# Optimization experiments

Measured on AMD Instinct MI355X. Metric: run time of the kernel, lower is better.

## Reference

```python
import jax, jax.numpy as jnp
import numpy as np

DIM = 512
NUM_HEADS = 8
DIM_HEAD = DIM // NUM_HEADS


def _xavier(key, shape):
    fan_in, fan_out = shape[0], shape[1]
    a = (6.0 / (fan_in + fan_out)) ** 0.5
    return jax.random.uniform(key, shape, jnp.float32, -a, a)


def setup_inputs() -> dict:
    key = jax.random.key(0)
    ks = jax.random.split(key, 8)
    B, N, M = 2, 2048, 2048
    x = jax.random.normal(ks[0], (B, N, DIM), jnp.float32)
    source = jax.random.normal(ks[1], (B, M, DIM), jnp.float32)
    source_mask = jax.random.randint(ks[2], (B, M), 0, 2) > 0
    Wq = _xavier(ks[3], (DIM, DIM)); bq = jnp.zeros((DIM,), jnp.float32)
    Wk = _xavier(ks[4], (DIM, DIM)); bk = jnp.zeros((DIM,), jnp.float32)
    Wv = _xavier(ks[5], (DIM, DIM)); bv = jnp.zeros((DIM,), jnp.float32)
    Wm = _xavier(ks[6], (DIM, DIM)); bm = jnp.zeros((DIM,), jnp.float32)
    return {"x": x, "source": source, "source_mask": source_mask,
            "Wq": Wq, "bq": bq, "Wk": Wk, "bk": bk,
            "Wv": Wv, "bv": bv, "Wm": Wm, "bm": bm}


def reference(x, source, source_mask, Wq, bq, Wk, bk, Wv, bv, Wm, bm):
    B, N, D = x.shape
    M = source.shape[-2]
    H, Dh = NUM_HEADS, DIM_HEAD
    # projections (torch Linear: x @ W^T + b)
    q = (x @ Wq.T + bq).reshape(B, N, H, Dh)
    k = (source @ Wk.T + bk).reshape(B, M, H, Dh)
    v = (source @ Wv.T + bv).reshape(B, M, H, Dh)
    scale = 1.0 / (Dh ** 0.5)
    # scores: [B, N, M, H]
    scores = jnp.einsum('bnhd,bmhd->bnmh', q, k) * scale
    scores = jnp.where(source_mask[:, None, :, None], scores, -jnp.inf)
    prob = jax.nn.softmax(scores, axis=-2)  # softmax over m
    agg = jnp.einsum('bnmh,bmhd->bnhd', prob, v).reshape(B, N, D)
    return agg @ Wm.T + bm
```

## Files before the change

kernel.cpp:

```cpp
#include <hip/hip_runtime.h>
#include <hip/hip_bf16.h>

#define DIMF 512
#define NHEAD 8
#define DHEAD 64
#define BATCH 2
#define SEQN 2048
#define SEQM 2048
#define FPS 40
#define QSCALE 0.18033688011112042f

typedef unsigned short u16;
typedef __attribute__((ext_vector_type(8))) short bf16x8;
typedef __attribute__((ext_vector_type(4))) float f32x4;

static __device__ __forceinline__ u16 f2bf(float f) {
    unsigned u = __float_as_uint(f);
    u += 0x7FFF + ((u >> 16) & 1);
    return (u16)(u >> 16);
}
static __device__ __forceinline__ u16 f2bf_fast(float f) {
    return (u16)((__float_as_uint(f) + 0x8000u) >> 16);
}

static __device__ __forceinline__
void load16(const u16* g, u16* l) {
    __builtin_amdgcn_global_load_lds(
        (const __attribute__((address_space(1))) void*)g,
        (__attribute__((address_space(3))) void*)l,
        16, 0, 0);
}

__global__ __launch_bounds__(256)
void cvt_w(const float* __restrict__ wq, const float* __restrict__ wk,
           const float* __restrict__ wv, const float* __restrict__ wm,
           const int* __restrict__ mask,
           u16* __restrict__ wqb, u16* __restrict__ wkb,
           u16* __restrict__ wvb, u16* __restrict__ wmb,
           u16* __restrict__ maskbf)
{
    int i = (blockIdx.x * 256 + threadIdx.x) * 4;
    if (blockIdx.y == 4) {
        if (i < BATCH * SEQM) {
            int4 m4 = *(const int4*)&mask[i];
            *(ushort4*)&maskbf[i] = make_ushort4(m4.x ? 0x3F80 : 0, m4.y ? 0x3F80 : 0,
                                                 m4.z ? 0x3F80 : 0, m4.w ? 0x3F80 : 0);
        }
        return;
    }
    const float* in = (blockIdx.y == 0) ? wq : (blockIdx.y == 1) ? wk
                    : (blockIdx.y == 2) ? wv : wm;
    u16* out = (blockIdx.y == 0) ? wqb : (blockIdx.y == 1) ? wkb
             : (blockIdx.y == 2) ? wvb : wmb;
    if (i >= DIMF * DIMF) return;
    float4 v = *(const float4*)&in[i];
    *(ushort4*)&out[i] = make_ushort4(f2bf(v.x), f2bf(v.y), f2bf(v.z), f2bf(v.w));
}

#define ASZ (64 * FPS)
#define BSZ (128 * FPS)

__device__ __forceinline__
void gemm_mfma(const float* __restrict__ Xf, const u16* __restrict__ Xb,
               const u16* __restrict__ W, const float* __restrict__ bias,
               const int* __restrict__ msk, void* __restrict__ Out, int mode)
{
    __shared__ __align__(16) u16 SH[2 * ASZ + 2 * BSZ];

    const int tid  = threadIdx.x;
    const int wave = tid >> 6;
    const int lane = tid & 63;
    const int l15  = lane & 15;
    const int quad = lane >> 4;
    const int wm = wave & 1, wn = wave >> 1;
    const int r0 = blockIdx.x * 64, c0 = blockIdx.y * 128;

    f32x4 acc[2][4] = {};

    const int br = tid >> 2, boct = tid & 3;
    const int ar = tid >> 3, aseg = tid & 7;

    bf16x8 rb0, rb1, rab;
    float4 ra0, ra1;

    auto loadg = [&](int k0) {
        rb0 = *(const bf16x8*)&W[(size_t)(c0 + br) * DIMF + k0 + boct * 8];
        rb1 = *(const bf16x8*)&W[(size_t)(c0 + br + 64) * DIMF + k0 + boct * 8];
        if (Xf) {
            ra0 = *(const float4*)&Xf[(size_t)(r0 + ar) * DIMF + k0 + aseg * 4];
            ra1 = *(const float4*)&Xf[(size_t)(r0 + ar + 32) * DIMF + k0 + aseg * 4];
        } else {
            rab = *(const bf16x8*)&Xb[(size_t)(r0 + br) * DIMF + k0 + boct * 8];
        }
    };
    auto stage = [&](int buf) {
        u16* As = SH + buf * ASZ;
        u16* Bs = SH + 2 * ASZ + buf * BSZ;
        if (Xf) {
            *(ushort4*)&As[ar * FPS + aseg * 4] =
                make_ushort4(f2bf(ra0.x), f2bf(ra0.y), f2bf(ra0.z), f2bf(ra0.w));
            *(ushort4*)&As[(ar + 32) * FPS + aseg * 4] =
                make_ushort4(f2bf(ra1.x), f2bf(ra1.y), f2bf(ra1.z), f2bf(ra1.w));
        } else {
            *(bf16x8*)&As[br * FPS + boct * 8] = rab;
        }
        *(bf16x8*)&Bs[br * FPS + boct * 8] = rb0;
        *(bf16x8*)&Bs[(br + 64) * FPS + boct * 8] = rb1;
    };

    loadg(0);
    stage(0);
    loadg(32);
    __syncthreads();

    const int NK = DIMF / 32;
    for (int kt = 0; kt < NK; ++kt) {
        const int cur = kt & 1;
        if (kt + 1 < NK) stage(cur ^ 1);
        if (kt + 2 < NK) loadg((kt + 2) * 32);
        const u16* As = SH + cur * ASZ;
        const u16* Bs = SH + 2 * ASZ + cur * BSZ;

        bf16x8 af[2], bf[4];
        #pragma unroll
        for (int mi = 0; mi < 2; ++mi)
            af[mi] = *(const bf16x8*)&As[(wm * 32 + mi * 16 + l15) * FPS + quad * 8];
        #pragma unroll
        for (int ni = 0; ni < 4; ++ni)
            bf[ni] = *(const bf16x8*)&Bs[(wn * 64 + ni * 16 + l15) * FPS + quad * 8];
        #pragma unroll
        for (int mi = 0; mi < 2; ++mi)
            #pragma unroll
            for (int ni = 0; ni < 4; ++ni)
                acc[mi][ni] = __builtin_amdgcn_mfma_f32_16x16x32_bf16(
                    af[mi], bf[ni], acc[mi][ni], 0, 0, 0);
        __syncthreads();
    }

    float bb[4];
    #pragma unroll
    for (int ni = 0; ni < 4; ++ni)
        bb[ni] = bias[c0 + wn * 64 + ni * 16 + l15];

    if (mode == 2) {
        u16* T = SH;
        const int b = r0 >> 11;
        const int n_base = r0 & (SEQN - 1);
        #pragma unroll
        for (int hh = 0; hh < 2; ++hh) {
            __syncthreads();
            if (wn == hh) {
                #pragma unroll
                for (int mi = 0; mi < 2; ++mi) {
                    const int rl = wm * 32 + mi * 16 + quad * 4;
                    int4 m4 = *(const int4*)&msk[b * SEQM + n_base + rl];
                    float mm[4];
                    mm[0] = m4.x ? 1.f : 0.f; mm[1] = m4.y ? 1.f : 0.f;
                    mm[2] = m4.z ? 1.f : 0.f; mm[3] = m4.w ? 1.f : 0.f;
                    #pragma unroll
                    for (int ni = 0; ni < 4; ++ni)
                        #pragma unroll
                        for (int r = 0; r < 4; ++r)
                            T[(rl + r) * 72 + ni * 16 + l15] =
                                f2bf((acc[mi][ni][r] + bb[ni]) * mm[r]);
                }
            }
            __syncthreads();
            const int d = tid >> 2, ms = (tid & 3) << 4;
            u16 tmp[16];
            #pragma unroll
            for (int j = 0; j < 16; ++j) tmp[j] = T[(ms + j) * 72 + d];
            const int hgl = (c0 >> 6) + hh;
            u16* dst = (u16*)Out + ((size_t)(b * NHEAD + hgl) * DHEAD + d) * SEQM
                       + n_base + ms;
            *(bf16x8*)&dst[0] = *(bf16x8*)&tmp[0];
            *(bf16x8*)&dst[8] = *(bf16x8*)&tmp[8];
        }
        return;
    }

    #pragma unroll
    for (int mi = 0; mi < 2; ++mi) {
        const int Rbase = r0 + wm * 32 + mi * 16 + quad * 4;
        const int b = Rbase >> 11;
        const int nb = Rbase & (SEQN - 1);
        #pragma unroll
        for (int ni = 0; ni < 4; ++ni) {
            const int C = c0 + wn * 64 + ni * 16 + l15;
            const int h = C >> 6, d = C & 63;
            if (mode == 0) {
                u16* ow = (u16*)Out;
                #pragma unroll
                for (int r = 0; r < 4; ++r)
                    ow[(((size_t)(b * NHEAD + h) * SEQN) + nb + r) * DHEAD + d] =
                        f2bf((acc[mi][ni][r] + bb[ni]) * QSCALE);
            } else if (mode == 1) {
                u16* ow = (u16*)Out;
                #pragma unroll
                for (int r = 0; r < 4; ++r)
                    ow[(((size_t)(b * NHEAD + h) * SEQN) + nb + r) * DHEAD + d] =
                        f2bf(acc[mi][ni][r] + bb[ni]);
            } else {
                float* ow = (float*)Out;
                #pragma unroll
                for (int r = 0; r < 4; ++r)
                    ow[(size_t)(Rbase + r) * DIMF + C] = acc[mi][ni][r] + bb[ni];
            }
        }
    }
}

__global__ __launch_bounds__(256, 3)
void qkv_proj(const float* __restrict__ x, const float* __restrict__ src,
              const u16* __restrict__ wqb, const float* __restrict__ bq,
              const u16* __restrict__ wkb, const float* __restrict__ bk,
              const u16* __restrict__ wvb, const float* __restrict__ bv,
              const int* __restrict__ mask,
              u16* __restrict__ qw, u16* __restrict__ kw, u16* __restrict__ vtw)
{
    const int z = blockIdx.z;
    const float* X = (z == 0) ? x : src;
    const u16* W = (z == 0) ? wqb : (z == 1) ? wkb : wvb;
    const float* B = (z == 0) ? bq : (z == 1) ? bk : bv;
    void* O = (z == 0) ? (void*)qw : (z == 1) ? (void*)kw : (void*)vtw;
    gemm_mfma(X, nullptr, W, B, mask, O, z);
}

__global__ __launch_bounds__(256, 3)
void out_proj(const u16* __restrict__ aggb, const u16* __restrict__ wmb,
              const float* __restrict__ bm, float* __restrict__ out)
{
    gemm_mfma(nullptr, aggb, wmb, bm, nullptr, (void*)out, 3);
}

__global__ __launch_bounds__(256, 2)
void flash_attn_mfma(const u16* __restrict__ q, const u16* __restrict__ k,
                     const u16* __restrict__ vt, const u16* __restrict__ maskbf,
                     u16* __restrict__ agg)
{
    __shared__ __align__(16) u16 KsD[2][4096];
    __shared__ __align__(16) u16 VtsD[2][4096];
    __shared__ u16 Ps[4 * 32 * FPS];
    float* Osum = (float*)&KsD[0][0];
    float* Lsum = (float*)&VtsD[0][0];

    const int tid  = threadIdx.x;
    const int wave = tid >> 6;
    const int lane = tid & 63;
    const int l15  = lane & 15;
    const int quad = lane >> 4;
    const int qg = wave >> 1, mh = wave & 1;

    const int bid  = blockIdx.x;
    const int xcd  = bid & 7, slot = bid >> 3;
    const int pair = (xcd << 1) | (slot & 1);
    const int b = pair >> 3, h = pair & 7;
    const int n0 = (slot >> 1) * 64;

    const size_t hoff = (size_t)(b * NHEAD + h) * (size_t)SEQM * DHEAD;
    const u16* kb = k  + hoff;
    const u16* vb = vt + hoff;
    const u16* mb = maskbf + b * SEQM;

    const int dr   = lane >> 3;
    const int doct = (lane & 7) ^ (dr & 7);
    const int g0 = wave, g1 = 4 + wave;
    const u16* kq0 = kb + (size_t)(g0 * 8 + dr) * DHEAD + doct * 8;
    const u16* kq1 = kb + (size_t)(g1 * 8 + dr) * DHEAD + doct * 8;
    const u16* vq0 = vb + (size_t)(g0 * 8 + dr) * SEQM + doct * 8;
    const u16* vq1 = vb + (size_t)(g1 * 8 + dr) * SEQM + doct * 8;

    bf16x8 qf[2][2];
    #pragma unroll
    for (int qh = 0; qh < 2; ++qh) {
        const u16* qp = q + hoff + (size_t)(n0 + qg * 32 + qh * 16 + l15) * DHEAD
                        + quad * 8;
        qf[qh][0] = *(const bf16x8*)qp;
        qf[qh][1] = *(const bf16x8*)(qp + 32);
    }

    load16(kq0, &KsD[0][g0 * 512]);
    load16(kq1, &KsD[0][g1 * 512]);
    load16(vq0, &VtsD[0][g0 * 512]);
    load16(vq1, &VtsD[0][g1 * 512]);
    bf16x8 mf_nxt = *(const bf16x8*)&mb[32 * mh + quad * 8];

    f32x4 O[2][4] = {};
    f32x4 lacc[2] = {};
    u16* Pw = Ps + wave * (32 * FPS);
    const int xoct = l15 & 7;

    for (int mt = 0; mt < SEQM / 64; ++mt) {
        const int cur = mt & 1;
        __syncthreads();
        bf16x8 mf = mf_nxt;
        if (mt + 1 < SEQM / 64) {
            const int m1 = (mt + 1) * 64;
            const int nb = cur ^ 1;
            load16(kq0 + (size_t)m1 * DHEAD, &KsD[nb][g0 * 512]);
            load16(kq1 + (size_t)m1 * DHEAD, &KsD[nb][g1 * 512]);
            load16(vq0 + m1, &VtsD[nb][g0 * 512]);
            load16(vq1 + m1, &VtsD[nb][g1 * 512]);
            mf_nxt = *(const bf16x8*)&mb[m1 + 32 * mh + quad * 8];
        }
        const u16* Ks  = KsD[cur];
        const u16* Vts = VtsD[cur];

        f32x4 st[2][2] = {};
        #pragma unroll
        for (int sub = 0; sub < 2; ++sub) {
            const int mrow = 32 * mh + 16 * sub + l15;
            #pragma unroll
            for (int c = 0; c < 2; ++c) {
                const int oct = (4 * c + quad) ^ xoct;
                bf16x8 af = *(const bf16x8*)&Ks[mrow * 64 + oct * 8];
                #pragma unroll
                for (int qh = 0; qh < 2; ++qh)
                    st[qh][sub] = __builtin_amdgcn_mfma_f32_16x16x32_bf16(
                        af, qf[qh][c], st[qh][sub], 0, 0, 0);
            }
        }

        #pragma unroll
        for (int qh = 0; qh < 2; ++qh)
            #pragma unroll
            for (int sub = 0; sub < 2; ++sub) {
                ushort4 w4 = make_ushort4(
                    f2bf_fast(__builtin_amdgcn_exp2f(st[qh][sub][0])),
                    f2bf_fast(__builtin_amdgcn_exp2f(st[qh][sub][1])),
                    f2bf_fast(__builtin_amdgcn_exp2f(st[qh][sub][2])),
                    f2bf_fast(__builtin_amdgcn_exp2f(st[qh][sub][3])));
                *(ushort4*)&Pw[(qh * 16 + l15) * FPS + 16 * sub + 4 * quad] = w4;
            }

        bf16x8 vf[4];
        #pragma unroll
        for (int sd = 0; sd < 4; ++sd) {
            const int oct = (4 * mh + quad) ^ xoct;
            vf[sd] = *(const bf16x8*)&Vts[(16 * sd + l15) * 64 + oct * 8];
        }

        #pragma unroll
        for (int qh = 0; qh < 2; ++qh) {
            bf16x8 pf = *(const bf16x8*)&Pw[(qh * 16 + l15) * FPS + quad * 8];
            lacc[qh] = __builtin_amdgcn_mfma_f32_16x16x32_bf16(pf, mf, lacc[qh], 0, 0, 0);
            #pragma unroll
            for (int sd = 0; sd < 4; ++sd)
                O[qh][sd] = __builtin_amdgcn_mfma_f32_16x16x32_bf16(
                    pf, vf[sd], O[qh][sd], 0, 0, 0);
        }
    }

    __syncthreads();
    if (mh == 1) {
        #pragma unroll
        for (int qh = 0; qh < 2; ++qh) {
            #pragma unroll
            for (int sd = 0; sd < 4; ++sd)
                #pragma unroll
                for (int r = 0; r < 4; ++r)
                    Osum[qg * 2048 + (qh * 16 + quad * 4 + r) * 64 + 16 * sd + l15]
                        = O[qh][sd][r];
            if (l15 == 0) {
                #pragma unroll
                for (int r = 0; r < 4; ++r)
                    Lsum[qg * 32 + qh * 16 + quad * 4 + r] = lacc[qh][r];
            }
        }
    }
    __syncthreads();
    if (mh == 0) {
        #pragma unroll
        for (int qh = 0; qh < 2; ++qh)
            #pragma unroll
            for (int r = 0; r < 4; ++r) {
                const float inv = 1.f /
                    (lacc[qh][r] + Lsum[qg * 32 + qh * 16 + quad * 4 + r]);
                const int n = n0 + qg * 32 + qh * 16 + quad * 4 + r;
                u16* ag = agg + ((size_t)b * SEQN + n) * DIMF + h * DHEAD + l15;
                #pragma unroll
                for (int sd = 0; sd < 4; ++sd)
                    ag[16 * sd] = f2bf((O[qh][sd][r] +
                        Osum[qg * 2048 + (qh * 16 + quad * 4 + r) * 64 + 16 * sd + l15])
                        * inv);
            }
    }
}

extern "C" void kernel_launch(void* const* d_in, const int* in_sizes, int n_in,
                              void* d_out, int out_size, void* d_ws, size_t ws_size,
                              hipStream_t stream)
{
    (void)in_sizes; (void)n_in; (void)out_size; (void)ws_size;
    const float* x      = (const float*)d_in[0];
    const float* source = (const float*)d_in[1];
    const int*   mask   = (const int*)  d_in[2];
    const float* Wq = (const float*)d_in[3]; const float* bq = (const float*)d_in[4];
    const float* Wk = (const float*)d_in[5]; const float* bk = (const float*)d_in[6];
    const float* Wv = (const float*)d_in[7]; const float* bv = (const float*)d_in[8];
    const float* Wm = (const float*)d_in[9]; const float* bm = (const float*)d_in[10];
    float* out = (float*)d_out;

    const size_t SZ = (size_t)BATCH * SEQN * DIMF;
    const size_t WZ = (size_t)DIMF * DIMF;
    u16* qw   = (u16*)d_ws;
    u16* kw   = qw  + SZ;
    u16* vtw  = kw  + SZ;
    u16* aggb = vtw + SZ;
    u16* wqb  = aggb + SZ;
    u16* wkb  = wqb + WZ;
    u16* wvb  = wkb + WZ;
    u16* wmb  = wvb + WZ;
    u16* maskbf = wmb + WZ;

    dim3 gcvt((WZ / 4 + 255) / 256, 5);
    cvt_w<<<gcvt, 256, 0, stream>>>(Wq, Wk, Wv, Wm, mask,
                                    wqb, wkb, wvb, wmb, maskbf);

    dim3 gproj(4096 / 64, 512 / 128, 3);
    qkv_proj<<<gproj, 256, 0, stream>>>(x, source, wqb, bq, wkb, bk, wvb, bv,
                                        mask, qw, kw, vtw);

    flash_attn_mfma<<<512, 256, 0, stream>>>(qw, kw, vtw, maskbf, aggb);

    dim3 gout(4096 / 64, 512 / 128);
    out_proj<<<gout, 256, 0, stream>>>(aggb, wmb, bm, out);
}
```

Before: 145.8 us.

## Triple-buffer K/V tiles in flash attention with explicit vmcnt waits

The attention kernel moves from double to triple buffering of K and Vt tiles in LDS. Loads run two tiles ahead, and each iteration waits only with a partial vmcnt on the oldest tile instead of a full __syncthreads drain. The projection GEMM also replaces __syncthreads with an lgkmcnt-only wait plus barrier. This hides global-load latency better, at the cost of more LDS (possibly lower occupancy) and hand-counted waitcnt values that must match the real number of outstanding loads.

```diff
diff --git a/kernel.cpp b/kernel.cpp
--- a/kernel.cpp
+++ b/kernel.cpp
@@ -30,6 +30,12 @@
         (__attribute__((address_space(3))) void*)l,
         16, 0, 0);
 }
+
+#define LDS_BARRIER() do {                                      \
+    asm volatile("s_waitcnt lgkmcnt(0)" ::: "memory");          \
+    __builtin_amdgcn_s_barrier();                               \
+    __builtin_amdgcn_sched_barrier(0);                          \
+} while (0)
 
 __global__ __launch_bounds__(256)
 void cvt_w(const float* __restrict__ wq, const float* __restrict__ wk,
@@ -111,7 +117,7 @@
     loadg(0);
     stage(0);
     loadg(32);
-    __syncthreads();
+    LDS_BARRIER();
 
     const int NK = DIMF / 32;
     for (int kt = 0; kt < NK; ++kt) {
@@ -134,7 +140,7 @@
             for (int ni = 0; ni < 4; ++ni)
                 acc[mi][ni] = __builtin_amdgcn_mfma_f32_16x16x32_bf16(
                     af[mi], bf[ni], acc[mi][ni], 0, 0, 0);
-        __syncthreads();
+        LDS_BARRIER();
     }
 
     float bb[4];
@@ -238,8 +244,8 @@
                      const u16* __restrict__ vt, const u16* __restrict__ maskbf,
                      u16* __restrict__ agg)
 {
-    __shared__ __align__(16) u16 KsD[2][4096];
-    __shared__ __align__(16) u16 VtsD[2][4096];
+    __shared__ __align__(16) u16 KsD[3][4096];
+    __shared__ __align__(16) u16 VtsD[3][4096];
     __shared__ u16 Ps[4 * 32 * FPS];
     float* Osum = (float*)&KsD[0][0];
     float* Lsum = (float*)&VtsD[0][0];
@@ -283,26 +289,37 @@
     load16(kq1, &KsD[0][g1 * 512]);
     load16(vq0, &VtsD[0][g0 * 512]);
     load16(vq1, &VtsD[0][g1 * 512]);
-    bf16x8 mf_nxt = *(const bf16x8*)&mb[32 * mh + quad * 8];
+    bf16x8 mf0 = *(const bf16x8*)&mb[32 * mh + quad * 8];
+    __builtin_amdgcn_sched_barrier(0);
+    load16(kq0 + (size_t)64 * DHEAD, &KsD[1][g0 * 512]);
+    load16(kq1 + (size_t)64 * DHEAD, &KsD[1][g1 * 512]);
+    load16(vq0 + 64, &VtsD[1][g0 * 512]);
+    load16(vq1 + 64, &VtsD[1][g1 * 512]);
+    bf16x8 mf1 = *(const bf16x8*)&mb[64 + 32 * mh + quad * 8];
+    __builtin_amdgcn_sched_barrier(0);
+    bf16x8 mf2 = {};
 
     f32x4 O[2][4] = {};
     f32x4 lacc[2] = {};
     u16* Pw = Ps + wave * (32 * FPS);
     const int xoct = l15 & 7;
-
-    for (int mt = 0; mt < SEQM / 64; ++mt) {
-        const int cur = mt & 1;
-        __syncthreads();
-        bf16x8 mf = mf_nxt;
-        if (mt + 1 < SEQM / 64) {
-            const int m1 = (mt + 1) * 64;
-            const int nb = cur ^ 1;
-            load16(kq0 + (size_t)m1 * DHEAD, &KsD[nb][g0 * 512]);
-            load16(kq1 + (size_t)m1 * DHEAD, &KsD[nb][g1 * 512]);
-            load16(vq0 + m1, &VtsD[nb][g0 * 512]);
-            load16(vq1 + m1, &VtsD[nb][g1 * 512]);
-            mf_nxt = *(const bf16x8*)&mb[m1 + 32 * mh + quad * 8];
-        }
+    const int NT = SEQM / 64;
+
+    int cur = 0, nx2 = 2;
+    for (int mt = 0; mt < NT; ++mt) {
+        if (mt < NT - 1) asm volatile("s_waitcnt vmcnt(5)" ::: "memory");
+        else             asm volatile("s_waitcnt vmcnt(0)" ::: "memory");
+        __builtin_amdgcn_s_barrier();
+        __builtin_amdgcn_sched_barrier(0);
+        if (mt + 2 < NT) {
+            const size_t m2 = (size_t)(mt + 2) * 64;
+            load16(kq0 + m2 * DHEAD, &KsD[nx2][g0 * 512]);
+            load16(kq1 + m2 * DHEAD, &KsD[nx2][g1 * 512]);
+            load16(vq0 + m2, &VtsD[nx2][g0 * 512]);
+            load16(vq1 + m2, &VtsD[nx2][g1 * 512]);
+            mf2 = *(const bf16x8*)&mb[m2 + 32 * mh + quad * 8];
+        }
+        bf16x8 mf = mf0; mf0 = mf1; mf1 = mf2;
         const u16* Ks  = KsD[cur];
         const u16* Vts = VtsD[cur];
 
@@ -349,6 +366,8 @@
                 O[qh][sd] = __builtin_amdgcn_mfma_f32_16x16x32_bf16(
                     pf, vf[sd], O[qh][sd], 0, 0, 0);
         }
+        cur = (cur == 2) ? 0 : cur + 1;
+        nx2 = (nx2 == 2) ? 0 : nx2 + 1;
     }
 
     __syncthreads();
```

Measured after the change: 149.1 us. 1.02x slower.

## Keep attention probabilities in registers via permlane swaps instead of LDS round-trip

Applied to the files above, without the earlier changes.

In the flash attention kernel, exp2 results are packed to bf16 with v_cvt_pk_bf16_f32 and rearranged across lanes with permlane32/permlane16 swaps to form the MFMA A-operand directly. This removes the per-wave LDS store/load of P and the Ps shared buffer. It also adds s_setprio around the MFMA blocks and replaces __syncthreads in the projection GEMM with an explicit lgkmcnt wait plus barrier. The lane permutation must exactly match the MFMA input layout, and the packed conversion rounds slightly differently from the old truncating helper.

```diff
diff --git a/kernel.cpp b/kernel.cpp
--- a/kernel.cpp
+++ b/kernel.cpp
@@ -19,9 +19,6 @@
     u += 0x7FFF + ((u >> 16) & 1);
     return (u16)(u >> 16);
 }
-static __device__ __forceinline__ u16 f2bf_fast(float f) {
-    return (u16)((__float_as_uint(f) + 0x8000u) >> 16);
-}
 
 static __device__ __forceinline__
 void load16(const u16* g, u16* l) {
@@ -30,6 +27,27 @@
         (__attribute__((address_space(3))) void*)l,
         16, 0, 0);
 }
+
+static __device__ __forceinline__
+void permpair(unsigned& a, unsigned& c) {
+#if __has_builtin(__builtin_amdgcn_permlane32_swap)
+    {
+        auto r1 = __builtin_amdgcn_permlane32_swap(a, c, false, false);
+        unsigned a1 = r1[0], c1 = r1[1];
+        auto r2 = __builtin_amdgcn_permlane16_swap(a1, c1, false, false);
+        a = r2[0]; c = r2[1];
+    }
+#else
+    asm("v_permlane32_swap_b32 %0, %1" : "+v"(a), "+v"(c));
+    asm("v_permlane16_swap_b32 %0, %1" : "+v"(a), "+v"(c));
+#endif
+}
+
+#define LDS_BARRIER() do {                                      \
+    asm volatile("s_waitcnt lgkmcnt(0)" ::: "memory");          \
+    __builtin_amdgcn_s_barrier();                               \
+    __builtin_amdgcn_sched_barrier(0);                          \
+} while (0)
 
 __global__ __launch_bounds__(256)
 void cvt_w(const float* __restrict__ wq, const float* __restrict__ wk,
@@ -111,7 +129,7 @@
     loadg(0);
     stage(0);
     loadg(32);
-    __syncthreads();
+    LDS_BARRIER();
 
     const int NK = DIMF / 32;
     for (int kt = 0; kt < NK; ++kt) {
@@ -134,7 +152,7 @@
             for (int ni = 0; ni < 4; ++ni)
                 acc[mi][ni] = __builtin_amdgcn_mfma_f32_16x16x32_bf16(
                     af[mi], bf[ni], acc[mi][ni], 0, 0, 0);
-        __syncthreads();
+        LDS_BARRIER();
     }
 
     float bb[4];
@@ -240,7 +258,6 @@
 {
     __shared__ __align__(16) u16 KsD[2][4096];
     __shared__ __align__(16) u16 VtsD[2][4096];
-    __shared__ u16 Ps[4 * 32 * FPS];
     float* Osum = (float*)&KsD[0][0];
     float* Lsum = (float*)&VtsD[0][0];
 
@@ -287,7 +304,6 @@
 
     f32x4 O[2][4] = {};
     f32x4 lacc[2] = {};
-    u16* Pw = Ps + wave * (32 * FPS);
     const int xoct = l15 & 7;
 
     for (int mt = 0; mt < SEQM / 64; ++mt) {
@@ -307,6 +323,7 @@
         const u16* Vts = VtsD[cur];
 
         f32x4 st[2][2] = {};
+        __builtin_amdgcn_s_setprio(1);
         #pragma unroll
         for (int sub = 0; sub < 2; ++sub) {
             const int mrow = 32 * mh + 16 * sub + l15;
@@ -320,18 +337,30 @@
                         af, qf[qh][c], st[qh][sub], 0, 0, 0);
             }
         }
-
-        #pragma unroll
-        for (int qh = 0; qh < 2; ++qh)
-            #pragma unroll
-            for (int sub = 0; sub < 2; ++sub) {
-                ushort4 w4 = make_ushort4(
-                    f2bf_fast(__builtin_amdgcn_exp2f(st[qh][sub][0])),
-                    f2bf_fast(__builtin_amdgcn_exp2f(st[qh][sub][1])),
-                    f2bf_fast(__builtin_amdgcn_exp2f(st[qh][sub][2])),
-                    f2bf_fast(__builtin_amdgcn_exp2f(st[qh][sub][3])));
-                *(ushort4*)&Pw[(qh * 16 + l15) * FPS + 16 * sub + 4 * quad] = w4;
-            }
+        __builtin_amdgcn_s_setprio(0);
+
+        bf16x8 pfr[2];
+        #pragma unroll
+        for (int qh = 0; qh < 2; ++qh) {
+            float e00 = __builtin_amdgcn_exp2f(st[qh][0][0]);
+            float e01 = __builtin_amdgcn_exp2f(st[qh][0][1]);
+            float e02 = __builtin_amdgcn_exp2f(st[qh][0][2]);
+            float e03 = __builtin_amdgcn_exp2f(st[qh][0][3]);
+            float e10 = __builtin_amdgcn_exp2f(st[qh][1][0]);
+            float e11 = __builtin_amdgcn_exp2f(st[qh][1][1]);
+            float e12 = __builtin_amdgcn_exp2f(st[qh][1][2]);
+            float e13 = __builtin_amdgcn_exp2f(st[qh][1][3]);
+            unsigned a0, a1, c0w, c1w;
+            asm("v_cvt_pk_bf16_f32 %0, %1, %2" : "=v"(a0)  : "v"(e00), "v"(e01));
+            asm("v_cvt_pk_bf16_f32 %0, %1, %2" : "=v"(a1)  : "v"(e02), "v"(e03));
+            asm("v_cvt_pk_bf16_f32 %0, %1, %2" : "=v"(c0w) : "v"(e10), "v"(e11));
+            asm("v_cvt_pk_bf16_f32 %0, %1, %2" : "=v"(c1w) : "v"(e12), "v"(e13));
+            permpair(a0, c0w);
+            permpair(a1, c1w);
+            union { unsigned u[4]; bf16x8 hv; } pu;
+            pu.u[0] = a0; pu.u[1] = a1; pu.u[2] = c0w; pu.u[3] = c1w;
+            pfr[qh] = pu.hv;
+        }
 
         bf16x8 vf[4];
         #pragma unroll
@@ -340,15 +369,17 @@
             vf[sd] = *(const bf16x8*)&Vts[(16 * sd + l15) * 64 + oct * 8];
         }
 
+        __builtin_amdgcn_s_setprio(1);
         #pragma unroll
         for (int qh = 0; qh < 2; ++qh) {
-            bf16x8 pf = *(const bf16x8*)&Pw[(qh * 16 + l15) * FPS + quad * 8];
-            lacc[qh] = __builtin_amdgcn_mfma_f32_16x16x32_bf16(pf, mf, lacc[qh], 0, 0, 0);
+            lacc[qh] = __builtin_amdgcn_mfma_f32_16x16x32_bf16(
+                pfr[qh], mf, lacc[qh], 0, 0, 0);
             #pragma unroll
             for (int sd = 0; sd < 4; ++sd)
                 O[qh][sd] = __builtin_amdgcn_mfma_f32_16x16x32_bf16(
-                    pf, vf[sd], O[qh][sd], 0, 0, 0);
-        }
+                    pfr[qh], vf[sd], O[qh][sd], 0, 0, 0);
+        }
+        __builtin_amdgcn_s_setprio(0);
     }
 
     __syncthreads();
```

Result: faster. 140.2 us (-3.9%).
